# Kernel optimization log

Measured on AMD Instinct MI355X. Metric: run time of the kernel, lower is better.

The kernel has to match this reference:

```python
import jax, jax.numpy as jnp
import numpy as np

T, C, H, W, D = 100, 2, 128, 128, 8192


def setup_inputs() -> dict:
    key = jax.random.key(0)
    k1, k2, k3, k4 = jax.random.split(key, 4)
    # event histogram: nonnegative intensities per (time, polarity, y, x)
    hist = jax.random.uniform(k1, (T, C, H, W), dtype=jnp.float32)
    # torchhd Random(vsa='MAP') tables are random bipolar {-1,+1} vectors
    time_w = jnp.sign(jax.random.normal(k2, (T, D), dtype=jnp.float32))
    pol_w = jnp.sign(jax.random.normal(k3, (C, D), dtype=jnp.float32))
    pos_w = jnp.sign(jax.random.normal(k4, (H * W, D), dtype=jnp.float32))
    return {"hist": hist, "time_w": time_w, "pol_w": pol_w, "pos_w": pos_w}


def reference(hist, time_w, pol_w, pos_w):
    # Original: for every nonzero pixel, bind (elementwise mul in MAP)
    # pos_hv * pol_hv * time_hv, scale by intensity, accumulate, then sign.
    # Equivalent fused form:
    #   out_d = sign( sum_{t,p,n} hist[t,p,n] * pos_w[n,d] * pol_w[p,d] * time_w[t,d] )
    t, c, h, w = hist.shape
    flat = hist.reshape(t, c, h * w)                      # [T, 2, H*W]
    # intensity-weighted sum of position HVs per (t, p): one GEMM over H*W
    acc = jnp.einsum('tpn,nd->tpd', flat, pos_w)          # [T, 2, D]
    # bind with polarity and time HVs, reduce over t and p
    gesture = jnp.einsum('tpd,pd,td->d', acc, pol_w, time_w)  # [D]
    return jnp.sign(gesture)
```

## Files before the change

kernel.cpp:

```cpp
#include <hip/hip_runtime.h>
#include <cstdint>
#include <cstddef>

#define TT    100
#define MROWS 200
#define KDIM  16384
#define DDIM  8192
#define KSL   16
#define KPER  (KDIM / KSL)

typedef __bf16 bf16x8 __attribute__((ext_vector_type(8)));
typedef float  f32x4  __attribute__((ext_vector_type(4)));

static __device__ __forceinline__ unsigned short f2bf_rne(float f) {
    unsigned int u = __float_as_uint(f);
    unsigned int r = (u + 0x7FFFu + ((u >> 16) & 1u)) >> 16;
    return (unsigned short)r;
}
static __device__ __forceinline__ float bf2f(unsigned short s) {
    return __uint_as_float(((unsigned int)s) << 16);
}

__global__ __launch_bounds__(256) void zero_kernel(float* __restrict__ out) {
    out[blockIdx.x * 256 + threadIdx.x] = 0.f;
}

__global__ __launch_bounds__(256) void gemm_kernel(const float* __restrict__ hist,
                                                   const float* __restrict__ pos,
                                                   const float* __restrict__ time_w,
                                                   const float* __restrict__ pol_w,
                                                   float* __restrict__ out) {
    __shared__ alignas(16) unsigned short As[2][128][32];
    __shared__ alignas(16) unsigned short Bs[128][40];
    __shared__ float sPart[128];

    const int t     = threadIdx.x;
    const int n0    = blockIdx.x * 128;
    const int m0    = blockIdx.y * 128;
    const int kbase = blockIdx.z * KPER;

    const int lane = t & 63;
    const int wv   = t >> 6;
    const int wm   = (wv & 1) * 64;
    const int wn   = (wv >> 1) * 64;
    const int l15  = lane & 15;
    const int q8   = (lane >> 4) * 8;

    if (t < 128) sPart[t] = 0.f;

    const int ar  = t >> 2;
    const int akb = (t & 3) * 8;
    const int rowA0 = m0 + ar;
    const int rowA1 = m0 + ar + 64;
    const bool v0 = rowA0 < MROWS;
    const bool v1 = rowA1 < MROWS;
    const float* gA0 = hist + (size_t)rowA0 * KDIM + akb;
    const float* gA1 = hist + (size_t)rowA1 * KDIM + akb;

    const int bk2 = (t & 15) * 2;
    const int bnb = (t >> 4) * 8;
    const float* gB0 = pos + ((size_t)kbase + bk2) * DDIM + n0 + bnb;
    const float* gB1 = gB0 + DDIM;

    f32x4 acc[4][4];
#pragma unroll
    for (int s = 0; s < 4; ++s)
#pragma unroll
        for (int j = 0; j < 4; ++j) acc[s][j] = (f32x4){0.f, 0.f, 0.f, 0.f};

    for (int kk = 0; kk < KPER; kk += 32) {
        float4 a00 = {0,0,0,0}, a01 = {0,0,0,0};
        float4 a10 = {0,0,0,0}, a11 = {0,0,0,0};
        if (v0) { a00 = *(const float4*)(gA0 + kbase + kk);
                  a01 = *(const float4*)(gA0 + kbase + kk + 4); }
        if (v1) { a10 = *(const float4*)(gA1 + kbase + kk);
                  a11 = *(const float4*)(gA1 + kbase + kk + 4); }
        const float* b0 = gB0 + (size_t)kk * DDIM;
        const float* b1 = gB1 + (size_t)kk * DDIM;
        float4 x0 = *(const float4*)(b0);
        float4 x1 = *(const float4*)(b0 + 4);
        float4 y0 = *(const float4*)(b1);
        float4 y1 = *(const float4*)(b1 + 4);

        __syncthreads();

        {
            float va[8] = {a00.x, a00.y, a00.z, a00.w, a01.x, a01.y, a01.z, a01.w};
            float vb[8] = {a10.x, a10.y, a10.z, a10.w, a11.x, a11.y, a11.z, a11.w};
            alignas(16) unsigned short h0[8], l0[8], h1[8], l1[8];
#pragma unroll
            for (int i = 0; i < 8; ++i) {
                unsigned short h = f2bf_rne(va[i]);
                h0[i] = h; l0[i] = f2bf_rne(va[i] - bf2f(h));
                unsigned short g = f2bf_rne(vb[i]);
                h1[i] = g; l1[i] = f2bf_rne(vb[i] - bf2f(g));
            }
            *(uint4*)&As[0][ar][akb]      = *(const uint4*)h0;
            *(uint4*)&As[1][ar][akb]      = *(const uint4*)l0;
            *(uint4*)&As[0][ar + 64][akb] = *(const uint4*)h1;
            *(uint4*)&As[1][ar + 64][akb] = *(const uint4*)l1;
        }
        {
            const float xv[8] = {x0.x, x0.y, x0.z, x0.w, x1.x, x1.y, x1.z, x1.w};
            const float yv[8] = {y0.x, y0.y, y0.z, y0.w, y1.x, y1.y, y1.z, y1.w};
#pragma unroll
            for (int j = 0; j < 8; ++j) {
                unsigned int w = (__float_as_uint(xv[j]) >> 16) |
                                 (__float_as_uint(yv[j]) & 0xFFFF0000u);
                *(unsigned int*)&Bs[bnb + j][bk2] = w;
            }
        }

        __syncthreads();

        uint4 fa0[4], fa1[4], fb[4];
#pragma unroll
        for (int s = 0; s < 4; ++s) {
            fa0[s] = *(const uint4*)&As[0][wm + s * 16 + l15][q8];
            fa1[s] = *(const uint4*)&As[1][wm + s * 16 + l15][q8];
        }
#pragma unroll
        for (int j = 0; j < 4; ++j)
            fb[j] = *(const uint4*)&Bs[wn + j * 16 + l15][q8];

#pragma unroll
        for (int s = 0; s < 4; ++s)
#pragma unroll
            for (int j = 0; j < 4; ++j) {
                acc[s][j] = __builtin_amdgcn_mfma_f32_16x16x32_bf16(
                    __builtin_bit_cast(bf16x8, fa0[s]),
                    __builtin_bit_cast(bf16x8, fb[j]), acc[s][j], 0, 0, 0);
                acc[s][j] = __builtin_amdgcn_mfma_f32_16x16x32_bf16(
                    __builtin_bit_cast(bf16x8, fa1[s]),
                    __builtin_bit_cast(bf16x8, fb[j]), acc[s][j], 0, 0, 0);
            }
    }

    const int qrow = (lane >> 4) * 4;
#pragma unroll
    for (int j = 0; j < 4; ++j) {
        const int col = wn + j * 16 + l15;
        const int d   = n0 + col;
        const float p0 = pol_w[d];
        const float p1 = pol_w[DDIM + d];
        float part = 0.f;
#pragma unroll
        for (int s = 0; s < 4; ++s)
#pragma unroll
            for (int r = 0; r < 4; ++r) {
                const int m = m0 + wm + s * 16 + qrow + r;
                if (m < MROWS) {
                    const int tt_ = m >> 1;
                    const float w = time_w[(size_t)tt_ * DDIM + d] *
                                    ((m & 1) ? p1 : p0);
                    part += w * acc[s][j][r];
                }
            }
        atomicAdd(&sPart[col], part);
    }
    __syncthreads();
    if (t < 128) atomicAdd(out + n0 + t, sPart[t]);
}

__global__ __launch_bounds__(256) void sign_kernel(float* __restrict__ out) {
    int d = blockIdx.x * 256 + threadIdx.x;
    float s = out[d];
    out[d] = (s > 0.f) ? 1.f : ((s < 0.f) ? -1.f : 0.f);
}

extern "C" void kernel_launch(void* const* d_in, const int* in_sizes, int n_in,
                              void* d_out, int out_size, void* d_ws, size_t ws_size,
                              hipStream_t stream) {
    const float* hist   = (const float*)d_in[0];
    const float* time_w = (const float*)d_in[1];
    const float* pol_w  = (const float*)d_in[2];
    const float* pos_w  = (const float*)d_in[3];
    float* out = (float*)d_out;
    (void)d_ws; (void)ws_size;

    zero_kernel<<<DDIM / 256, 256, 0, stream>>>(out);
    gemm_kernel<<<dim3(DDIM / 128, 2, KSL), 256, 0, stream>>>(hist, pos_w, time_w, pol_w, out);
    sign_kernel<<<DDIM / 256, 256, 0, stream>>>(out);
}
```

Baseline: 768.3 us.

## Prefetch next K tile into registers during MFMA and simplify bf16 split

Global loads for the next K-slice are issued right after the LDS barrier, so they are in flight while the MFMAs run. The hi/lo bf16 split and B packing happen after the MFMAs, and their results are written to LDS at the start of the next iteration. The split rounding is simplified to round-half-up with masking. The B load pattern now uses two float4s 64 columns apart, and launch bounds request two blocks per CU. In exchange, register pressure rises, one redundant wrap-around load happens on the last iteration, and rounding differs slightly from RNE.

```diff
diff --git a/kernel.cpp b/kernel.cpp
--- a/kernel.cpp
+++ b/kernel.cpp
@@ -12,24 +12,33 @@
 typedef __bf16 bf16x8 __attribute__((ext_vector_type(8)));
 typedef float  f32x4  __attribute__((ext_vector_type(4)));
 
-static __device__ __forceinline__ unsigned short f2bf_rne(float f) {
-    unsigned int u = __float_as_uint(f);
-    unsigned int r = (u + 0x7FFFu + ((u >> 16) & 1u)) >> 16;
-    return (unsigned short)r;
-}
-static __device__ __forceinline__ float bf2f(unsigned short s) {
-    return __uint_as_float(((unsigned int)s) << 16);
-}
-
 __global__ __launch_bounds__(256) void zero_kernel(float* __restrict__ out) {
     out[blockIdx.x * 256 + threadIdx.x] = 0.f;
 }
 
-__global__ __launch_bounds__(256) void gemm_kernel(const float* __restrict__ hist,
-                                                   const float* __restrict__ pos,
-                                                   const float* __restrict__ time_w,
-                                                   const float* __restrict__ pol_w,
-                                                   float* __restrict__ out) {
+static __device__ __forceinline__ void split_row(const float4 a, const float4 b,
+                                                 uint4& hi, uint4& lo) {
+    const float v[8] = {a.x, a.y, a.z, a.w, b.x, b.y, b.z, b.w};
+    unsigned int h[8];
+    unsigned int m[8];
+#pragma unroll
+    for (int i = 0; i < 8; ++i) {
+        unsigned int u = __float_as_uint(v[i]);
+        h[i] = (u + 0x8000u) & 0xFFFF0000u;
+        float l = v[i] - __uint_as_float(h[i]);
+        m[i] = (__float_as_uint(l) + 0x8000u) & 0xFFFF0000u;
+    }
+    hi.x = (h[0] >> 16) | h[1];  hi.y = (h[2] >> 16) | h[3];
+    hi.z = (h[4] >> 16) | h[5];  hi.w = (h[6] >> 16) | h[7];
+    lo.x = (m[0] >> 16) | m[1];  lo.y = (m[2] >> 16) | m[3];
+    lo.z = (m[4] >> 16) | m[5];  lo.w = (m[6] >> 16) | m[7];
+}
+
+__global__ __launch_bounds__(256, 2) void gemm_kernel(const float* __restrict__ hist,
+                                                      const float* __restrict__ pos,
+                                                      const float* __restrict__ time_w,
+                                                      const float* __restrict__ pol_w,
+                                                      float* __restrict__ out) {
     __shared__ alignas(16) unsigned short As[2][128][32];
     __shared__ alignas(16) unsigned short Bs[128][40];
     __shared__ float sPart[128];
@@ -50,17 +59,15 @@
 
     const int ar  = t >> 2;
     const int akb = (t & 3) * 8;
-    const int rowA0 = m0 + ar;
-    const int rowA1 = m0 + ar + 64;
-    const bool v0 = rowA0 < MROWS;
-    const bool v1 = rowA1 < MROWS;
-    const float* gA0 = hist + (size_t)rowA0 * KDIM + akb;
-    const float* gA1 = hist + (size_t)rowA1 * KDIM + akb;
-
-    const int bk2 = (t & 15) * 2;
-    const int bnb = (t >> 4) * 8;
-    const float* gB0 = pos + ((size_t)kbase + bk2) * DDIM + n0 + bnb;
-    const float* gB1 = gB0 + DDIM;
+    const bool v0 = (m0 + ar)      < MROWS;
+    const bool v1 = (m0 + ar + 64) < MROWS;
+    const float* gA0 = hist + (size_t)(m0 + ar)      * KDIM + akb + kbase;
+    const float* gA1 = hist + (size_t)(m0 + ar + 64) * KDIM + akb + kbase;
+
+    const int bp = t & 15;
+    const int bq = t >> 4;
+    const float* gB0 = pos + ((size_t)kbase + 2 * bp)     * DDIM + n0 + 4 * bq;
+    const float* gB1 = pos + ((size_t)kbase + 2 * bp + 1) * DDIM + n0 + 4 * bq;
 
     f32x4 acc[4][4];
 #pragma unroll
@@ -68,50 +75,55 @@
 #pragma unroll
         for (int j = 0; j < 4; ++j) acc[s][j] = (f32x4){0.f, 0.f, 0.f, 0.f};
 
+    float4 a00 = {0,0,0,0}, a01 = {0,0,0,0}, a10 = {0,0,0,0}, a11 = {0,0,0,0};
+    if (v0) { a00 = *(const float4*)(gA0);     a01 = *(const float4*)(gA0 + 4); }
+    if (v1) { a10 = *(const float4*)(gA1);     a11 = *(const float4*)(gA1 + 4); }
+    float4 bx0 = *(const float4*)(gB0);
+    float4 bx1 = *(const float4*)(gB0 + 64);
+    float4 by0 = *(const float4*)(gB1);
+    float4 by1 = *(const float4*)(gB1 + 64);
+
+    uint4 wAh0, wAl0, wAh1, wAl1;
+    unsigned int wB[8];
+    split_row(a00, a01, wAh0, wAl0);
+    split_row(a10, a11, wAh1, wAl1);
+    {
+        const float x0[4] = {bx0.x, bx0.y, bx0.z, bx0.w};
+        const float x1[4] = {bx1.x, bx1.y, bx1.z, bx1.w};
+        const float y0[4] = {by0.x, by0.y, by0.z, by0.w};
+        const float y1[4] = {by1.x, by1.y, by1.z, by1.w};
+#pragma unroll
+        for (int j = 0; j < 4; ++j) {
+            wB[j]     = (__float_as_uint(x0[j]) >> 16) |
+                        (__float_as_uint(y0[j]) & 0xFFFF0000u);
+            wB[4 + j] = (__float_as_uint(x1[j]) >> 16) |
+                        (__float_as_uint(y1[j]) & 0xFFFF0000u);
+        }
+    }
+
     for (int kk = 0; kk < KPER; kk += 32) {
-        float4 a00 = {0,0,0,0}, a01 = {0,0,0,0};
-        float4 a10 = {0,0,0,0}, a11 = {0,0,0,0};
-        if (v0) { a00 = *(const float4*)(gA0 + kbase + kk);
-                  a01 = *(const float4*)(gA0 + kbase + kk + 4); }
-        if (v1) { a10 = *(const float4*)(gA1 + kbase + kk);
-                  a11 = *(const float4*)(gA1 + kbase + kk + 4); }
-        const float* b0 = gB0 + (size_t)kk * DDIM;
-        const float* b1 = gB1 + (size_t)kk * DDIM;
-        float4 x0 = *(const float4*)(b0);
-        float4 x1 = *(const float4*)(b0 + 4);
-        float4 y0 = *(const float4*)(b1);
-        float4 y1 = *(const float4*)(b1 + 4);
-
         __syncthreads();
 
-        {
-            float va[8] = {a00.x, a00.y, a00.z, a00.w, a01.x, a01.y, a01.z, a01.w};
-            float vb[8] = {a10.x, a10.y, a10.z, a10.w, a11.x, a11.y, a11.z, a11.w};
-            alignas(16) unsigned short h0[8], l0[8], h1[8], l1[8];
-#pragma unroll
-            for (int i = 0; i < 8; ++i) {
-                unsigned short h = f2bf_rne(va[i]);
-                h0[i] = h; l0[i] = f2bf_rne(va[i] - bf2f(h));
-                unsigned short g = f2bf_rne(vb[i]);
-                h1[i] = g; l1[i] = f2bf_rne(vb[i] - bf2f(g));
-            }
-            *(uint4*)&As[0][ar][akb]      = *(const uint4*)h0;
-            *(uint4*)&As[1][ar][akb]      = *(const uint4*)l0;
-            *(uint4*)&As[0][ar + 64][akb] = *(const uint4*)h1;
-            *(uint4*)&As[1][ar + 64][akb] = *(const uint4*)l1;
-        }
-        {
-            const float xv[8] = {x0.x, x0.y, x0.z, x0.w, x1.x, x1.y, x1.z, x1.w};
-            const float yv[8] = {y0.x, y0.y, y0.z, y0.w, y1.x, y1.y, y1.z, y1.w};
-#pragma unroll
-            for (int j = 0; j < 8; ++j) {
-                unsigned int w = (__float_as_uint(xv[j]) >> 16) |
-                                 (__float_as_uint(yv[j]) & 0xFFFF0000u);
-                *(unsigned int*)&Bs[bnb + j][bk2] = w;
-            }
+        *(uint4*)&As[0][ar][akb]      = wAh0;
+        *(uint4*)&As[1][ar][akb]      = wAl0;
+        *(uint4*)&As[0][ar + 64][akb] = wAh1;
+        *(uint4*)&As[1][ar + 64][akb] = wAl1;
+#pragma unroll
+        for (int j = 0; j < 4; ++j) {
+            *(unsigned int*)&Bs[4 * bq + j][2 * bp]      = wB[j];
+            *(unsigned int*)&Bs[64 + 4 * bq + j][2 * bp] = wB[4 + j];
         }
 
         __syncthreads();
+
+        const int kn = (kk + 32 < KPER) ? kk + 32 : 0;
+        a00 = (float4){0,0,0,0}; a01 = a00; a10 = a00; a11 = a00;
+        if (v0) { a00 = *(const float4*)(gA0 + kn);     a01 = *(const float4*)(gA0 + kn + 4); }
+        if (v1) { a10 = *(const float4*)(gA1 + kn);     a11 = *(const float4*)(gA1 + kn + 4); }
+        bx0 = *(const float4*)(gB0 + (size_t)kn * DDIM);
+        bx1 = *(const float4*)(gB0 + (size_t)kn * DDIM + 64);
+        by0 = *(const float4*)(gB1 + (size_t)kn * DDIM);
+        by1 = *(const float4*)(gB1 + (size_t)kn * DDIM + 64);
 
         uint4 fa0[4], fa1[4], fb[4];
 #pragma unroll
@@ -134,6 +146,22 @@
                     __builtin_bit_cast(bf16x8, fa1[s]),
                     __builtin_bit_cast(bf16x8, fb[j]), acc[s][j], 0, 0, 0);
             }
+
+        split_row(a00, a01, wAh0, wAl0);
+        split_row(a10, a11, wAh1, wAl1);
+        {
+            const float x0[4] = {bx0.x, bx0.y, bx0.z, bx0.w};
+            const float x1[4] = {bx1.x, bx1.y, bx1.z, bx1.w};
+            const float y0[4] = {by0.x, by0.y, by0.z, by0.w};
+            const float y1[4] = {by1.x, by1.y, by1.z, by1.w};
+#pragma unroll
+            for (int j = 0; j < 4; ++j) {
+                wB[j]     = (__float_as_uint(x0[j]) >> 16) |
+                            (__float_as_uint(y0[j]) & 0xFFFF0000u);
+                wB[4 + j] = (__float_as_uint(x1[j]) >> 16) |
+                            (__float_as_uint(y1[j]) & 0xFFFF0000u);
+            }
+        }
     }
 
     const int qrow = (lane >> 4) * 4;
```

After: 845.7 us. 10.1% more time.
